# Kernel optimization log

Measured on AMD Instinct MI355X. Metric: run time of the kernel, lower is better.

## Reference

```python
import jax, jax.numpy as jnp
import numpy as np

N = 50000   # nodes
E = 600000  # edges
D = 128     # emb_dim
L = 5       # num_layers
ATOM_DIMS = np.array([119, 4, 11, 13, 11, 7, 13, 2, 9]) + 5   # per-feature vocab (+5 as in source)
BOND_DIMS = np.array([7, 22, 2]) + 5
BL_CENTERS = np.arange(0.0, 2.0, 0.1, dtype=np.float32)   # 20 centers, gamma 10
PR_CENTERS = np.arange(0.0, 1.0, 0.05, dtype=np.float32)  # 20 centers, gamma 1
BL_GAMMA = 10.0
PR_GAMMA = 1.0
BN_EPS = 1e-5


def setup_inputs() -> dict:
    key = jax.random.key(0)
    ks = jax.random.split(key, 16)
    scale = 1.0 / np.sqrt(D)
    atom_off = jnp.asarray(np.concatenate([[0], np.cumsum(ATOM_DIMS)[:-1]]), jnp.int32)
    bond_off = jnp.asarray(np.concatenate([[0], np.cumsum(BOND_DIMS)[:-1]]), jnp.int32)
    return {
        "x": jax.random.randint(ks[0], (N, 9), 0, 7, dtype=jnp.int32),
        "edge_index": jax.random.randint(ks[1], (2, E), 0, N, dtype=jnp.int32),
        "edge_attr_int": jax.random.randint(ks[2], (E, 3), 0, 7, dtype=jnp.int32),
        "edge_attr_float": jax.random.uniform(ks[3], (E, 2), dtype=jnp.float32),
        "atom_off": atom_off,
        "bond_off": bond_off,
        "atom_emb": jax.random.normal(ks[4], (int(ATOM_DIMS.sum()), D), jnp.float32) * scale,
        "bond_emb": jax.random.normal(ks[5], (L, int(BOND_DIMS.sum()), D), jnp.float32) * scale,
        "W_bl": jax.random.normal(ks[6], (L, len(BL_CENTERS), D), jnp.float32) * scale,
        "b_bl": jnp.zeros((L, D), jnp.float32),
        "W_pr": jax.random.normal(ks[7], (L, len(PR_CENTERS), D), jnp.float32) * scale,
        "b_pr": jnp.zeros((L, D), jnp.float32),
        "mlp_W1": jax.random.normal(ks[8], (L, D, D), jnp.float32) * scale,
        "mlp_b1": jnp.zeros((L, D), jnp.float32),
        "bn1_g": jnp.ones((L, D), jnp.float32),
        "bn1_b": jnp.zeros((L, D), jnp.float32),
        "mlp_W2": jax.random.normal(ks[9], (L, D, D), jnp.float32) * scale,
        "mlp_b2": jnp.zeros((L, D), jnp.float32),
        "eps_gin": jnp.zeros((L,), jnp.float32),
        "bn_g": jnp.ones((L, D), jnp.float32),
        "bn_b": jnp.zeros((L, D), jnp.float32),
    }


def _bn(h, g, b):
    # BatchNorm1d, training-mode batch statistics over the node axis
    m = h.mean(0)
    v = h.var(0)
    return (h - m) * jax.lax.rsqrt(v + BN_EPS) * g + b


def _rbf(x, centers, gamma):
    # exp(-gamma * (x - c)^2): [E] -> [E, n_centers]
    return jnp.exp(-gamma * jnp.square(x[:, None] - centers[None, :]))


def reference(x, edge_index, edge_attr_int, edge_attr_float, atom_off, bond_off,
              atom_emb, bond_emb, W_bl, b_bl, W_pr, b_pr,
              mlp_W1, mlp_b1, bn1_g, bn1_b, mlp_W2, mlp_b2,
              eps_gin, bn_g, bn_b):
    # AtomEncoder: sum of 9 categorical embeddings (flat table + offsets)
    h = atom_emb[x + atom_off[None, :]].sum(1)  # [N, D]
    src, dst = edge_index[0], edge_index[1]
    bl = _rbf(edge_attr_float[:, 0], jnp.asarray(BL_CENTERS), BL_GAMMA)  # [E, 20]
    pr = _rbf(edge_attr_float[:, 1], jnp.asarray(PR_CENTERS), PR_GAMMA)  # [E, 20]
    for l in range(L):
        # per-layer edge embedding: BondEncoder + BondFloatRBF
        e = bond_emb[l][edge_attr_int + bond_off[None, :]].sum(1)
        e = e + bl @ W_bl[l] + b_bl[l] + pr @ W_pr[l] + b_pr[l]
        # GINConv (aggr='add'): mlp((1+eps)*x + sum_j relu(x_j + e_ij))
        msg = jax.nn.relu(h[src] + e)                       # [E, D]
        agg = jax.ops.segment_sum(msg, dst, num_segments=N)  # [N, D]
        z = (1.0 + eps_gin[l]) * h + agg
        z = z @ mlp_W1[l] + mlp_b1[l]
        z = jax.nn.relu(_bn(z, bn1_g[l], bn1_b[l]))
        z = z @ mlp_W2[l] + mlp_b2[l]
        # outer per-layer BatchNorm; ReLU except last layer (drop_ratio=0)
        z = _bn(z, bn_g[l], bn_b[l])
        if l < L - 1:
            z = jax.nn.relu(z)
        h = z
    return h  # JK='last'
```

## Files before the change

### kernel.cpp

```cpp
#include <hip/hip_runtime.h>
#include <hip/hip_bf16.h>

#define GN 50000
#define GE 600000
#define DD 128
#define TQ 4096
#define NBOND 2268
#define TROWS (2*(TQ+1) + NBOND)
#define SCB 49
#define NBANK 64
#define SSET (NBANK*256)

typedef __attribute__((ext_vector_type(8))) short short8;
typedef __attribute__((ext_vector_type(4))) float floatx4;

__device__ __forceinline__ unsigned short f2b(float f) {
    __hip_bfloat16 h = __float2bfloat16(f);
    return __builtin_bit_cast(unsigned short, h);
}
__device__ __forceinline__ float b2f_lo(unsigned int u) { return __uint_as_float(u << 16); }
__device__ __forceinline__ float b2f_hi(unsigned int u) { return __uint_as_float(u & 0xffff0000u); }
__device__ __forceinline__ float bs2f(short s) {
    return __uint_as_float(((unsigned int)(unsigned short)s) << 16);
}

__global__ __launch_bounds__(256) void atom_kernel(
    const int* __restrict__ x, const int* __restrict__ atom_off,
    const float* __restrict__ atom_emb, unsigned short* __restrict__ h)
{
    int t = blockIdx.x * 256 + threadIdx.x;
    if (t >= GN * DD) return;
    int n = t >> 7, d = t & 127;
    float s = 0.f;
#pragma unroll
    for (int f = 0; f < 9; f++) {
        int idx = x[n * 9 + f] + atom_off[f];
        s += atom_emb[idx * DD + d];
    }
    h[t] = f2b(s);
}

__global__ __launch_bounds__(256) void hist_kernel(const int* __restrict__ ei, int* __restrict__ count)
{
    int e = blockIdx.x * 256 + threadIdx.x;
    if (e < GE) atomicAdd(&count[ei[GE + e]], 1);
}

__global__ __launch_bounds__(1024) void scan1_kernel(
    const int* __restrict__ count, int* __restrict__ row_start, int* __restrict__ blocksum)
{
    __shared__ int sh[1024];
    int t = threadIdx.x;
    int idx = blockIdx.x * 1024 + t;
    int v = (idx < GN) ? count[idx] : 0;
    sh[t] = v;
    __syncthreads();
    for (int off = 1; off < 1024; off <<= 1) {
        int u = (t >= off) ? sh[t - off] : 0;
        __syncthreads();
        sh[t] += u;
        __syncthreads();
    }
    if (idx <= GN) row_start[idx] = (t == 0) ? 0 : sh[t - 1];
    if (t == 1023) blocksum[blockIdx.x] = sh[1023];
}

__global__ __launch_bounds__(64) void scan2_kernel(
    const int* __restrict__ blocksum, int* __restrict__ blockoff)
{
    int t = threadIdx.x;
    int v = (t < SCB) ? blocksum[t] : 0;
#pragma unroll
    for (int off = 1; off < 64; off <<= 1) {
        int u = __shfl_up(v, off);
        if (t >= off) v += u;
    }
    int e = __shfl_up(v, 1);
    if (t == 0) e = 0;
    if (t < SCB) blockoff[t] = e;
}

__global__ __launch_bounds__(1024) void scan3_kernel(
    int* __restrict__ row_start, const int* __restrict__ blockoff)
{
    int idx = blockIdx.x * 1024 + threadIdx.x;
    if (idx <= GN) row_start[idx] += blockoff[blockIdx.x];
}

__global__ __launch_bounds__(256) void scatter_kernel(
    const int* __restrict__ ei, const int* __restrict__ eai, const float* __restrict__ eaf,
    const int* __restrict__ row_start, int* __restrict__ fill, int4* __restrict__ ep)
{
    int e = blockIdx.x * 256 + threadIdx.x;
    if (e < GE) {
        int d = ei[GE + e];
        int p = row_start[d] + atomicAdd(&fill[d], 1);
        int src = ei[e];
        float x1 = eaf[2 * e], x2 = eaf[2 * e + 1];
        int q1 = (int)(x1 * (float)TQ + 0.5f); q1 = min(max(q1, 0), TQ);
        int q2 = (int)(x2 * (float)TQ + 0.5f); q2 = min(max(q2, 0), TQ);
        int b0 = eai[3 * e], b1 = eai[3 * e + 1], b2 = eai[3 * e + 2];
        ep[p] = make_int4(src, q1 | (q2 << 16), (b0 * 27 + b1) * 7 + b2, 0);
    }
}

__global__ __launch_bounds__(128) void tables_kernel(
    const float* __restrict__ W_bl, const float* __restrict__ b_bl,
    const float* __restrict__ W_pr, const float* __restrict__ b_pr,
    const float* __restrict__ bond_emb, const int* __restrict__ bond_off,
    unsigned short* __restrict__ tbl_bl, unsigned short* __restrict__ tbl_pr,
    unsigned short* __restrict__ tbl_bond)
{
    int l = blockIdx.x / TROWS;
    int b = blockIdx.x % TROWS;
    int d = threadIdx.x;
    const float* W_bl_l = W_bl + (size_t)l * 20 * DD;
    const float* W_pr_l = W_pr + (size_t)l * 20 * DD;
    const float* bemb_l = bond_emb + (size_t)l * 46 * DD;
    if (b < (TQ + 1)) {
        float xq = b * (1.0f / TQ);
        float s = b_bl[(size_t)l * DD + d] + b_pr[(size_t)l * DD + d];
#pragma unroll
        for (int k = 0; k < 20; k++) {
            float dl = xq - 0.1f * k;
            s += __expf(-10.f * dl * dl) * W_bl_l[k * DD + d];
        }
        tbl_bl[((size_t)l * (TQ + 1) + b) * DD + d] = f2b(s);
    } else if (b < 2 * (TQ + 1)) {
        int q = b - (TQ + 1);
        float xq = q * (1.0f / TQ);
        float s = 0.f;
#pragma unroll
        for (int k = 0; k < 20; k++) {
            float dl = xq - 0.05f * k;
            s += __expf(-dl * dl) * W_pr_l[k * DD + d];
        }
        tbl_pr[((size_t)l * (TQ + 1) + q) * DD + d] = f2b(s);
    } else {
        int r = b - 2 * (TQ + 1);
        int b0 = r / 189;
        int rem = r % 189;
        int b1 = rem / 7, b2 = rem % 7;
        tbl_bond[((size_t)l * NBOND + r) * DD + d] =
            f2b(bemb_l[(b0 + bond_off[0]) * DD + d]
              + bemb_l[(b1 + bond_off[1]) * DD + d]
              + bemb_l[(b2 + bond_off[2]) * DD + d]);
    }
}

__global__ __launch_bounds__(256) void wfrag_kernel(
    const float* __restrict__ W1, const float* __restrict__ W2,
    unsigned short* __restrict__ wf_hi, unsigned short* __restrict__ wf_lo)
{
    int t = blockIdx.x * 256 + threadIdx.x;
    if (t >= 10 * 2048) return;
    int mat = t >> 11;
    int rem = t & 2047;
    int kt = rem >> 9;
    int rem2 = rem & 511;
    int nt = rem2 >> 6;
    int lane = rem2 & 63;
    const float* src = (mat & 1) ? (W2 + (size_t)(mat >> 1) * DD * DD)
                                 : (W1 + (size_t)(mat >> 1) * DD * DD);
    int n = nt * 16 + (lane & 15);
    int k0 = kt * 32 + (lane >> 4) * 8;
    size_t base = (size_t)mat * 16384 + (size_t)((kt * 8 + nt) * 64 + lane) * 8;
#pragma unroll
    for (int j = 0; j < 8; j++) {
        float w = src[(size_t)(k0 + j) * DD + n];
        unsigned short hi = f2b(w);
        wf_hi[base + j] = hi;
        wf_lo[base + j] = f2b(w - bs2f((short)hi));
    }
}

__global__ __launch_bounds__(256) void edge_kernel(
    const int4* __restrict__ ep,
    const unsigned short* __restrict__ tbl_bl, const unsigned short* __restrict__ tbl_pr,
    const unsigned short* __restrict__ tbl_bond,
    const unsigned short* __restrict__ h, const int* __restrict__ row_start,
    const float* __restrict__ eps_gin, int layer,
    float* __restrict__ A)
{
    int tid = threadIdx.x;
    int wid = __builtin_amdgcn_readfirstlane(tid >> 6);
    int lane = tid & 63;
    int n = blockIdx.x * 4 + wid;
    int s0 = __builtin_amdgcn_readfirstlane(row_start[n]);
    int s1 = __builtin_amdgcn_readfirstlane(row_start[n + 1]);
    const unsigned int* hu = (const unsigned int*)h;
    const unsigned int* tb = (const unsigned int*)tbl_bl;
    const unsigned int* tp = (const unsigned int*)tbl_pr;
    const unsigned int* tg = (const unsigned int*)tbl_bond;
    float a0 = 0.f, a1 = 0.f;
    int p = s0;
    for (; p + 2 <= s1; p += 2) {
        int4 m0 = ep[p];
        int4 m1 = ep[p + 1];
        unsigned int ub0 = tb[(size_t)(m0.y & 0xffff) * 64 + lane];
        unsigned int up0 = tp[(size_t)((unsigned)m0.y >> 16) * 64 + lane];
        unsigned int ug0 = tg[(size_t)m0.z * 64 + lane];
        unsigned int uh0 = hu[(size_t)m0.x * 64 + lane];
        unsigned int ub1 = tb[(size_t)(m1.y & 0xffff) * 64 + lane];
        unsigned int up1 = tp[(size_t)((unsigned)m1.y >> 16) * 64 + lane];
        unsigned int ug1 = tg[(size_t)m1.z * 64 + lane];
        unsigned int uh1 = hu[(size_t)m1.x * 64 + lane];
        a0 += fmaxf(b2f_lo(uh0) + b2f_lo(ub0) + b2f_lo(up0) + b2f_lo(ug0), 0.f);
        a1 += fmaxf(b2f_hi(uh0) + b2f_hi(ub0) + b2f_hi(up0) + b2f_hi(ug0), 0.f);
        a0 += fmaxf(b2f_lo(uh1) + b2f_lo(ub1) + b2f_lo(up1) + b2f_lo(ug1), 0.f);
        a1 += fmaxf(b2f_hi(uh1) + b2f_hi(ub1) + b2f_hi(up1) + b2f_hi(ug1), 0.f);
    }
    if (p < s1) {
        int4 m0 = ep[p];
        unsigned int ub0 = tb[(size_t)(m0.y & 0xffff) * 64 + lane];
        unsigned int up0 = tp[(size_t)((unsigned)m0.y >> 16) * 64 + lane];
        unsigned int ug0 = tg[(size_t)m0.z * 64 + lane];
        unsigned int uh0 = hu[(size_t)m0.x * 64 + lane];
        a0 += fmaxf(b2f_lo(uh0) + b2f_lo(ub0) + b2f_lo(up0) + b2f_lo(ug0), 0.f);
        a1 += fmaxf(b2f_hi(uh0) + b2f_hi(ub0) + b2f_hi(up0) + b2f_hi(ug0), 0.f);
    }
    float eps1 = 1.f + eps_gin[layer];
    unsigned int un = hu[(size_t)n * 64 + lane];
    a0 += eps1 * b2f_lo(un);
    a1 += eps1 * b2f_hi(un);
    float2 o; o.x = a0; o.y = a1;
    *(float2*)(A + (size_t)n * DD + 2 * lane) = o;
}

template <int MODE>
__global__ __launch_bounds__(256) void gemm_kernel(
    const float* __restrict__ Asrc,
    const unsigned short* __restrict__ wf_hi, const unsigned short* __restrict__ wf_lo,
    const float* __restrict__ bias, float* __restrict__ Cdst,
    const float* __restrict__ stats_in, const float* __restrict__ bn_g,
    const float* __restrict__ bn_b, float* __restrict__ stats_out)
{
    __shared__ float sc_s[DD], tr_s[DD];
    __shared__ float red_s[4][DD];
    __shared__ float red_q[4][DD];
    int tid = threadIdx.x, wid = tid >> 6, lane = tid & 63;
    if (MODE == 1) {
        if (tid < DD) {
            float s = 0.f, q = 0.f;
#pragma unroll
            for (int bk = 0; bk < NBANK; bk++) {
                s += stats_in[bk * 256 + tid];
                q += stats_in[bk * 256 + 128 + tid];
            }
            float m = s * (1.0f / GN);
            float v = q * (1.0f / GN) - m * m;
            float sc = bn_g[tid] * rsqrtf(v + 1e-5f);
            sc_s[tid] = sc;
            tr_s[tid] = bn_b[tid] - m * sc;
        }
        __syncthreads();
    }
    int quad = lane >> 4, l16 = lane & 15;
    int row = blockIdx.x * 64 + wid * 16 + l16;
    bool rvalid = row < GN;

    floatx4 acc[8];
#pragma unroll
    for (int nt = 0; nt < 8; nt++) acc[nt] = (floatx4){0.f, 0.f, 0.f, 0.f};

    const short8* bhp = (const short8*)wf_hi;
    const short8* blp = (const short8*)wf_lo;
#pragma unroll
    for (int kt = 0; kt < 4; kt++) {
        short8 ahi = {0,0,0,0,0,0,0,0}, alo = {0,0,0,0,0,0,0,0};
        if (rvalid) {
            const float* ap = Asrc + (size_t)row * DD + kt * 32 + quad * 8;
            float a[8];
            *(float4*)(a)     = *(const float4*)(ap);
            *(float4*)(a + 4) = *(const float4*)(ap + 4);
            if (MODE == 1) {
                int kb = kt * 32 + quad * 8;
#pragma unroll
                for (int j = 0; j < 8; j++)
                    a[j] = fmaxf(a[j] * sc_s[kb + j] + tr_s[kb + j], 0.f);
            }
#pragma unroll
            for (int j = 0; j < 8; j++) {
                unsigned short hi = f2b(a[j]);
                ahi[j] = (short)hi;
                alo[j] = (short)f2b(a[j] - bs2f((short)hi));
            }
        }
#pragma unroll
        for (int nt = 0; nt < 8; nt++) {
            short8 bhi = bhp[(kt * 8 + nt) * 64 + lane];
            short8 blo = blp[(kt * 8 + nt) * 64 + lane];
            acc[nt] = __builtin_amdgcn_mfma_f32_16x16x32_bf16(ahi, bhi, acc[nt], 0, 0, 0);
            acc[nt] = __builtin_amdgcn_mfma_f32_16x16x32_bf16(alo, bhi, acc[nt], 0, 0, 0);
            acc[nt] = __builtin_amdgcn_mfma_f32_16x16x32_bf16(ahi, blo, acc[nt], 0, 0, 0);
        }
    }

#pragma unroll
    for (int nt = 0; nt < 8; nt++) {
        int col = nt * 16 + l16;
        float bv = bias[col];
        float s = 0.f, q = 0.f;
#pragma unroll
        for (int v = 0; v < 4; v++) {
            int r = blockIdx.x * 64 + wid * 16 + quad * 4 + v;
            float o = acc[nt][v] + bv;
            if (r < GN) {
                s += o; q += o * o;
                Cdst[(size_t)r * DD + col] = o;
            }
        }
        s += __shfl_xor(s, 16); s += __shfl_xor(s, 32);
        q += __shfl_xor(q, 16); q += __shfl_xor(q, 32);
        if (lane < 16) { red_s[wid][col] = s; red_q[wid][col] = q; }
    }
    __syncthreads();
    int bank = blockIdx.x & (NBANK - 1);
    if (tid < DD) {
        float s = red_s[0][tid] + red_s[1][tid] + red_s[2][tid] + red_s[3][tid];
        atomicAdd(&stats_out[bank * 256 + tid], s);
    } else {
        int c = tid - DD;
        float q = red_q[0][c] + red_q[1][c] + red_q[2][c] + red_q[3][c];
        atomicAdd(&stats_out[bank * 256 + 128 + c], q);
    }
}

__global__ __launch_bounds__(256) void bn_apply_kernel(
    const float* __restrict__ Z, const float* __restrict__ stats2,
    const float* __restrict__ g, const float* __restrict__ b,
    unsigned short* __restrict__ hout, float* __restrict__ fout, int last)
{
    __shared__ float sc_s[DD], tr_s[DD];
    int tid = threadIdx.x;
    if (tid < DD) {
        float s = 0.f, q = 0.f;
#pragma unroll
        for (int bk = 0; bk < NBANK; bk++) {
            s += stats2[bk * 256 + tid];
            q += stats2[bk * 256 + 128 + tid];
        }
        float m = s * (1.0f / GN);
        float v = q * (1.0f / GN) - m * m;
        float sc = g[tid] * rsqrtf(v + 1e-5f);
        sc_s[tid] = sc;
        tr_s[tid] = b[tid] - m * sc;
    }
    __syncthreads();
    const int total = GN * DD;
    for (int t = blockIdx.x * 256 + tid; t < total; t += gridDim.x * 256) {
        int c = t & 127;
        float val = Z[t] * sc_s[c] + tr_s[c];
        if (last) fout[t] = val;
        else      hout[t] = f2b(fmaxf(val, 0.f));
    }
}

extern "C" void kernel_launch(void* const* d_in, const int* in_sizes, int n_in,
                              void* d_out, int out_size, void* d_ws, size_t ws_size,
                              hipStream_t stream)
{
    const int*   x        = (const int*)d_in[0];
    const int*   ei       = (const int*)d_in[1];
    const int*   eai      = (const int*)d_in[2];
    const float* eaf      = (const float*)d_in[3];
    const int*   atom_off = (const int*)d_in[4];
    const int*   bond_off = (const int*)d_in[5];
    const float* atom_emb = (const float*)d_in[6];
    const float* bond_emb = (const float*)d_in[7];
    const float* W_bl     = (const float*)d_in[8];
    const float* b_bl     = (const float*)d_in[9];
    const float* W_pr     = (const float*)d_in[10];
    const float* b_pr     = (const float*)d_in[11];
    const float* W1       = (const float*)d_in[12];
    const float* b1       = (const float*)d_in[13];
    const float* bn1g     = (const float*)d_in[14];
    const float* bn1b     = (const float*)d_in[15];
    const float* W2       = (const float*)d_in[16];
    const float* b2       = (const float*)d_in[17];
    const float* eps_gin  = (const float*)d_in[18];
    const float* bng      = (const float*)d_in[19];
    const float* bnb      = (const float*)d_in[20];
    float* out = (float*)d_out;

    char* p = (char*)d_ws;
    unsigned short* h_bf  = (unsigned short*)p;  p += (size_t)GN * DD * 2;
    float* A              = (float*)p;           p += (size_t)GN * DD * 4;
    float* z1             = (float*)p;           p += (size_t)GN * DD * 4;
    unsigned short* tbl_bl   = (unsigned short*)p;  p += (size_t)5 * (TQ + 1) * DD * 2;
    unsigned short* tbl_pr   = (unsigned short*)p;  p += (size_t)5 * (TQ + 1) * DD * 2;
    unsigned short* tbl_bond = (unsigned short*)p;  p += (size_t)5 * NBOND * DD * 2;
    unsigned short* wf_hi    = (unsigned short*)p;  p += (size_t)10 * 16384 * 2;
    unsigned short* wf_lo    = (unsigned short*)p;  p += (size_t)10 * 16384 * 2;
    float* stats_all = (float*)p;  p += (size_t)10 * SSET * 4;
    int* count    = (int*)p;    p += (size_t)GN * 4;
    int* fill     = (int*)p;    p += (size_t)GN * 4;
    int* row_start= (int*)p;    p += (size_t)(GN + 1) * 4;
    int* blocksum = (int*)p;    p += (size_t)SCB * 4;
    int* blockoff = (int*)p;    p += (size_t)SCB * 4;
    p = (char*)(((size_t)p + 15) & ~(size_t)15);
    int4* ep      = (int4*)p;   p += (size_t)GE * 16;

    hipMemsetAsync(count, 0, (size_t)GN * 4, stream);
    hipMemsetAsync(fill,  0, (size_t)GN * 4, stream);
    hipMemsetAsync(stats_all, 0, (size_t)10 * SSET * 4, stream);

    hist_kernel<<<(GE + 255) / 256, 256, 0, stream>>>(ei, count);
    scan1_kernel<<<SCB, 1024, 0, stream>>>(count, row_start, blocksum);
    scan2_kernel<<<1, 64, 0, stream>>>(blocksum, blockoff);
    scan3_kernel<<<SCB, 1024, 0, stream>>>(row_start, blockoff);
    scatter_kernel<<<(GE + 255) / 256, 256, 0, stream>>>(ei, eai, eaf, row_start, fill, ep);
    atom_kernel<<<(GN * DD + 255) / 256, 256, 0, stream>>>(x, atom_off, atom_emb, h_bf);
    wfrag_kernel<<<80, 256, 0, stream>>>(W1, W2, wf_hi, wf_lo);
    tables_kernel<<<5 * TROWS, 128, 0, stream>>>(
        W_bl, b_bl, W_pr, b_pr, bond_emb, bond_off, tbl_bl, tbl_pr, tbl_bond);

    for (int l = 0; l < 5; l++) {
        float* stats1 = stats_all + (size_t)(2 * l + 0) * SSET;
        float* stats2 = stats_all + (size_t)(2 * l + 1) * SSET;

        edge_kernel<<<GN / 4, 256, 0, stream>>>(
            ep,
            tbl_bl + (size_t)l * (TQ + 1) * DD,
            tbl_pr + (size_t)l * (TQ + 1) * DD,
            tbl_bond + (size_t)l * NBOND * DD,
            h_bf, row_start, eps_gin, l, A);

        gemm_kernel<0><<<(GN + 63) / 64, 256, 0, stream>>>(
            A, wf_hi + (size_t)(l * 2 + 0) * 16384, wf_lo + (size_t)(l * 2 + 0) * 16384,
            b1 + (size_t)l * DD, z1, nullptr, nullptr, nullptr, stats1);

        gemm_kernel<1><<<(GN + 63) / 64, 256, 0, stream>>>(
            z1, wf_hi + (size_t)(l * 2 + 1) * 16384, wf_lo + (size_t)(l * 2 + 1) * 16384,
            b2 + (size_t)l * DD, A,
            stats1, bn1g + (size_t)l * DD, bn1b + (size_t)l * DD, stats2);

        bn_apply_kernel<<<1024, 256, 0, stream>>>(
            A, stats2, bng + (size_t)l * DD, bnb + (size_t)l * DD,
            h_bf, out, (l == 4) ? 1 : 0);
    }
}
```

Measured before the change: 773.2 us.

## Fuse edge aggregation with first MLP GEMM via LDS-staged tile

Merges the per-node edge aggregation kernel and the first MLP GEMM into one kernel. Each 256-thread block aggregates 64 node rows into an LDS tile, then runs the split-bf16 MFMA GEMM on it, writes z1 and accumulates BN statistics. This removes the fp32 A round trip through global memory and one launch per layer. In exchange, each wave processes 16 nodes serially and the grid shrinks from 12500 to 782 blocks, which may lower the latency hiding available to the gather. NBANK drops from 64 to 16 and the templated gemm is simplified to its single remaining mode.

```diff
diff --git a/kernel.cpp b/kernel.cpp
--- a/kernel.cpp
+++ b/kernel.cpp
@@ -8,8 +8,10 @@
 #define NBOND 2268
 #define TROWS (2*(TQ+1) + NBOND)
 #define SCB 49
-#define NBANK 64
+#define NBANK 16
 #define SSET (NBANK*256)
+#define NB 782
+#define LDA 132
 
 typedef __attribute__((ext_vector_type(8))) short short8;
 typedef __attribute__((ext_vector_type(4))) float floatx4;
@@ -174,60 +176,130 @@
     }
 }
 
-__global__ __launch_bounds__(256) void edge_kernel(
+__global__ __launch_bounds__(256) void edge_gemm_kernel(
     const int4* __restrict__ ep,
     const unsigned short* __restrict__ tbl_bl, const unsigned short* __restrict__ tbl_pr,
     const unsigned short* __restrict__ tbl_bond,
     const unsigned short* __restrict__ h, const int* __restrict__ row_start,
     const float* __restrict__ eps_gin, int layer,
-    float* __restrict__ A)
-{
+    const unsigned short* __restrict__ wf_hi, const unsigned short* __restrict__ wf_lo,
+    const float* __restrict__ bias, float* __restrict__ Cdst, float* __restrict__ stats_out)
+{
+    __shared__ float At[64 * LDA];
+    __shared__ float red_s[4][DD];
+    __shared__ float red_q[4][DD];
     int tid = threadIdx.x;
     int wid = __builtin_amdgcn_readfirstlane(tid >> 6);
     int lane = tid & 63;
-    int n = blockIdx.x * 4 + wid;
-    int s0 = __builtin_amdgcn_readfirstlane(row_start[n]);
-    int s1 = __builtin_amdgcn_readfirstlane(row_start[n + 1]);
+
     const unsigned int* hu = (const unsigned int*)h;
     const unsigned int* tb = (const unsigned int*)tbl_bl;
     const unsigned int* tp = (const unsigned int*)tbl_pr;
     const unsigned int* tg = (const unsigned int*)tbl_bond;
-    float a0 = 0.f, a1 = 0.f;
-    int p = s0;
-    for (; p + 2 <= s1; p += 2) {
-        int4 m0 = ep[p];
-        int4 m1 = ep[p + 1];
-        unsigned int ub0 = tb[(size_t)(m0.y & 0xffff) * 64 + lane];
-        unsigned int up0 = tp[(size_t)((unsigned)m0.y >> 16) * 64 + lane];
-        unsigned int ug0 = tg[(size_t)m0.z * 64 + lane];
-        unsigned int uh0 = hu[(size_t)m0.x * 64 + lane];
-        unsigned int ub1 = tb[(size_t)(m1.y & 0xffff) * 64 + lane];
-        unsigned int up1 = tp[(size_t)((unsigned)m1.y >> 16) * 64 + lane];
-        unsigned int ug1 = tg[(size_t)m1.z * 64 + lane];
-        unsigned int uh1 = hu[(size_t)m1.x * 64 + lane];
-        a0 += fmaxf(b2f_lo(uh0) + b2f_lo(ub0) + b2f_lo(up0) + b2f_lo(ug0), 0.f);
-        a1 += fmaxf(b2f_hi(uh0) + b2f_hi(ub0) + b2f_hi(up0) + b2f_hi(ug0), 0.f);
-        a0 += fmaxf(b2f_lo(uh1) + b2f_lo(ub1) + b2f_lo(up1) + b2f_lo(ug1), 0.f);
-        a1 += fmaxf(b2f_hi(uh1) + b2f_hi(ub1) + b2f_hi(up1) + b2f_hi(ug1), 0.f);
-    }
-    if (p < s1) {
-        int4 m0 = ep[p];
-        unsigned int ub0 = tb[(size_t)(m0.y & 0xffff) * 64 + lane];
-        unsigned int up0 = tp[(size_t)((unsigned)m0.y >> 16) * 64 + lane];
-        unsigned int ug0 = tg[(size_t)m0.z * 64 + lane];
-        unsigned int uh0 = hu[(size_t)m0.x * 64 + lane];
-        a0 += fmaxf(b2f_lo(uh0) + b2f_lo(ub0) + b2f_lo(up0) + b2f_lo(ug0), 0.f);
-        a1 += fmaxf(b2f_hi(uh0) + b2f_hi(ub0) + b2f_hi(up0) + b2f_hi(ug0), 0.f);
-    }
     float eps1 = 1.f + eps_gin[layer];
-    unsigned int un = hu[(size_t)n * 64 + lane];
-    a0 += eps1 * b2f_lo(un);
-    a1 += eps1 * b2f_hi(un);
-    float2 o; o.x = a0; o.y = a1;
-    *(float2*)(A + (size_t)n * DD + 2 * lane) = o;
-}
-
-template <int MODE>
+    for (int i = 0; i < 16; i++) {
+        int rl = wid * 16 + i;
+        int n = blockIdx.x * 64 + rl;
+        float a0 = 0.f, a1 = 0.f;
+        if (n < GN) {
+            int s0 = __builtin_amdgcn_readfirstlane(row_start[n]);
+            int s1 = __builtin_amdgcn_readfirstlane(row_start[n + 1]);
+            int p = s0;
+            for (; p + 2 <= s1; p += 2) {
+                int4 m0 = ep[p];
+                int4 m1 = ep[p + 1];
+                unsigned int ub0 = tb[(size_t)(m0.y & 0xffff) * 64 + lane];
+                unsigned int up0 = tp[(size_t)((unsigned)m0.y >> 16) * 64 + lane];
+                unsigned int ug0 = tg[(size_t)m0.z * 64 + lane];
+                unsigned int uh0 = hu[(size_t)m0.x * 64 + lane];
+                unsigned int ub1 = tb[(size_t)(m1.y & 0xffff) * 64 + lane];
+                unsigned int up1 = tp[(size_t)((unsigned)m1.y >> 16) * 64 + lane];
+                unsigned int ug1 = tg[(size_t)m1.z * 64 + lane];
+                unsigned int uh1 = hu[(size_t)m1.x * 64 + lane];
+                a0 += fmaxf(b2f_lo(uh0) + b2f_lo(ub0) + b2f_lo(up0) + b2f_lo(ug0), 0.f);
+                a1 += fmaxf(b2f_hi(uh0) + b2f_hi(ub0) + b2f_hi(up0) + b2f_hi(ug0), 0.f);
+                a0 += fmaxf(b2f_lo(uh1) + b2f_lo(ub1) + b2f_lo(up1) + b2f_lo(ug1), 0.f);
+                a1 += fmaxf(b2f_hi(uh1) + b2f_hi(ub1) + b2f_hi(up1) + b2f_hi(ug1), 0.f);
+            }
+            if (p < s1) {
+                int4 m0 = ep[p];
+                unsigned int ub0 = tb[(size_t)(m0.y & 0xffff) * 64 + lane];
+                unsigned int up0 = tp[(size_t)((unsigned)m0.y >> 16) * 64 + lane];
+                unsigned int ug0 = tg[(size_t)m0.z * 64 + lane];
+                unsigned int uh0 = hu[(size_t)m0.x * 64 + lane];
+                a0 += fmaxf(b2f_lo(uh0) + b2f_lo(ub0) + b2f_lo(up0) + b2f_lo(ug0), 0.f);
+                a1 += fmaxf(b2f_hi(uh0) + b2f_hi(ub0) + b2f_hi(up0) + b2f_hi(ug0), 0.f);
+            }
+            unsigned int un = hu[(size_t)n * 64 + lane];
+            a0 += eps1 * b2f_lo(un);
+            a1 += eps1 * b2f_hi(un);
+        }
+        float2 o; o.x = a0; o.y = a1;
+        *(float2*)(&At[rl * LDA + 2 * lane]) = o;
+    }
+    __syncthreads();
+
+    int quad = lane >> 4, l16 = lane & 15;
+    int rl2 = wid * 16 + l16;
+    floatx4 acc[8];
+#pragma unroll
+    for (int nt = 0; nt < 8; nt++) acc[nt] = (floatx4){0.f, 0.f, 0.f, 0.f};
+
+    const short8* bhp = (const short8*)wf_hi;
+    const short8* blp = (const short8*)wf_lo;
+#pragma unroll
+    for (int kt = 0; kt < 4; kt++) {
+        const float* ap = At + rl2 * LDA + kt * 32 + quad * 8;
+        float a[8];
+        *(float4*)(a)     = *(const float4*)(ap);
+        *(float4*)(a + 4) = *(const float4*)(ap + 4);
+        short8 ahi, alo;
+#pragma unroll
+        for (int j = 0; j < 8; j++) {
+            unsigned short hi = f2b(a[j]);
+            ahi[j] = (short)hi;
+            alo[j] = (short)f2b(a[j] - bs2f((short)hi));
+        }
+#pragma unroll
+        for (int nt = 0; nt < 8; nt++) {
+            short8 bhi = bhp[(kt * 8 + nt) * 64 + lane];
+            short8 blo = blp[(kt * 8 + nt) * 64 + lane];
+            acc[nt] = __builtin_amdgcn_mfma_f32_16x16x32_bf16(ahi, bhi, acc[nt], 0, 0, 0);
+            acc[nt] = __builtin_amdgcn_mfma_f32_16x16x32_bf16(alo, bhi, acc[nt], 0, 0, 0);
+            acc[nt] = __builtin_amdgcn_mfma_f32_16x16x32_bf16(ahi, blo, acc[nt], 0, 0, 0);
+        }
+    }
+
+#pragma unroll
+    for (int nt = 0; nt < 8; nt++) {
+        int col = nt * 16 + l16;
+        float bv = bias[col];
+        float s = 0.f, q = 0.f;
+#pragma unroll
+        for (int v = 0; v < 4; v++) {
+            int r = blockIdx.x * 64 + wid * 16 + quad * 4 + v;
+            float o = acc[nt][v] + bv;
+            if (r < GN) {
+                s += o; q += o * o;
+                Cdst[(size_t)r * DD + col] = o;
+            }
+        }
+        s += __shfl_xor(s, 16); s += __shfl_xor(s, 32);
+        q += __shfl_xor(q, 16); q += __shfl_xor(q, 32);
+        if (lane < 16) { red_s[wid][col] = s; red_q[wid][col] = q; }
+    }
+    __syncthreads();
+    int bank = blockIdx.x & (NBANK - 1);
+    if (tid < DD) {
+        float s = red_s[0][tid] + red_s[1][tid] + red_s[2][tid] + red_s[3][tid];
+        atomicAdd(&stats_out[bank * 256 + tid], s);
+    } else {
+        int c = tid - DD;
+        float q = red_q[0][c] + red_q[1][c] + red_q[2][c] + red_q[3][c];
+        atomicAdd(&stats_out[bank * 256 + 128 + c], q);
+    }
+}
+
 __global__ __launch_bounds__(256) void gemm_kernel(
     const float* __restrict__ Asrc,
     const unsigned short* __restrict__ wf_hi, const unsigned short* __restrict__ wf_lo,
@@ -239,22 +311,20 @@
     __shared__ float red_s[4][DD];
     __shared__ float red_q[4][DD];
     int tid = threadIdx.x, wid = tid >> 6, lane = tid & 63;
-    if (MODE == 1) {
-        if (tid < DD) {
-            float s = 0.f, q = 0.f;
-#pragma unroll
-            for (int bk = 0; bk < NBANK; bk++) {
-                s += stats_in[bk * 256 + tid];
-                q += stats_in[bk * 256 + 128 + tid];
-            }
-            float m = s * (1.0f / GN);
-            float v = q * (1.0f / GN) - m * m;
-            float sc = bn_g[tid] * rsqrtf(v + 1e-5f);
-            sc_s[tid] = sc;
-            tr_s[tid] = bn_b[tid] - m * sc;
-        }
-        __syncthreads();
-    }
+    if (tid < DD) {
+        float s = 0.f, q = 0.f;
+#pragma unroll
+        for (int bk = 0; bk < NBANK; bk++) {
+            s += stats_in[bk * 256 + tid];
+            q += stats_in[bk * 256 + 128 + tid];
+        }
+        float m = s * (1.0f / GN);
+        float v = q * (1.0f / GN) - m * m;
+        float sc = bn_g[tid] * rsqrtf(v + 1e-5f);
+        sc_s[tid] = sc;
+        tr_s[tid] = bn_b[tid] - m * sc;
+    }
+    __syncthreads();
     int quad = lane >> 4, l16 = lane & 15;
     int row = blockIdx.x * 64 + wid * 16 + l16;
     bool rvalid = row < GN;
@@ -273,12 +343,10 @@
             float a[8];
             *(float4*)(a)     = *(const float4*)(ap);
             *(float4*)(a + 4) = *(const float4*)(ap + 4);
-            if (MODE == 1) {
-                int kb = kt * 32 + quad * 8;
-#pragma unroll
-                for (int j = 0; j < 8; j++)
-                    a[j] = fmaxf(a[j] * sc_s[kb + j] + tr_s[kb + j], 0.f);
-            }
+            int kb = kt * 32 + quad * 8;
+#pragma unroll
+            for (int j = 0; j < 8; j++)
+                a[j] = fmaxf(a[j] * sc_s[kb + j] + tr_s[kb + j], 0.f);
 #pragma unroll
             for (int j = 0; j < 8; j++) {
                 unsigned short hi = f2b(a[j]);
@@ -385,8 +453,8 @@
 
     char* p = (char*)d_ws;
     unsigned short* h_bf  = (unsigned short*)p;  p += (size_t)GN * DD * 2;
-    float* A              = (float*)p;           p += (size_t)GN * DD * 4;
     float* z1             = (float*)p;           p += (size_t)GN * DD * 4;
+    float* z2             = (float*)p;           p += (size_t)GN * DD * 4;
     unsigned short* tbl_bl   = (unsigned short*)p;  p += (size_t)5 * (TQ + 1) * DD * 2;
     unsigned short* tbl_pr   = (unsigned short*)p;  p += (size_t)5 * (TQ + 1) * DD * 2;
     unsigned short* tbl_bond = (unsigned short*)p;  p += (size_t)5 * NBOND * DD * 2;
@@ -419,24 +487,22 @@
         float* stats1 = stats_all + (size_t)(2 * l + 0) * SSET;
         float* stats2 = stats_all + (size_t)(2 * l + 1) * SSET;
 
-        edge_kernel<<<GN / 4, 256, 0, stream>>>(
+        edge_gemm_kernel<<<NB, 256, 0, stream>>>(
             ep,
             tbl_bl + (size_t)l * (TQ + 1) * DD,
             tbl_pr + (size_t)l * (TQ + 1) * DD,
             tbl_bond + (size_t)l * NBOND * DD,
-            h_bf, row_start, eps_gin, l, A);
-
-        gemm_kernel<0><<<(GN + 63) / 64, 256, 0, stream>>>(
-            A, wf_hi + (size_t)(l * 2 + 0) * 16384, wf_lo + (size_t)(l * 2 + 0) * 16384,
-            b1 + (size_t)l * DD, z1, nullptr, nullptr, nullptr, stats1);
-
-        gemm_kernel<1><<<(GN + 63) / 64, 256, 0, stream>>>(
+            h_bf, row_start, eps_gin, l,
+            wf_hi + (size_t)(l * 2 + 0) * 16384, wf_lo + (size_t)(l * 2 + 0) * 16384,
+            b1 + (size_t)l * DD, z1, stats1);
+
+        gemm_kernel<<<NB, 256, 0, stream>>>(
             z1, wf_hi + (size_t)(l * 2 + 1) * 16384, wf_lo + (size_t)(l * 2 + 1) * 16384,
-            b2 + (size_t)l * DD, A,
+            b2 + (size_t)l * DD, z2,
             stats1, bn1g + (size_t)l * DD, bn1b + (size_t)l * DD, stats2);
 
         bn_apply_kernel<<<1024, 256, 0, stream>>>(
-            A, stats2, bng + (size_t)l * DD, bnb + (size_t)l * DD,
+            z2, stats2, bng + (size_t)l * DD, bnb + (size_t)l * DD,
             h_bf, out, (l == 4) ? 1 : 0);
     }
 }
```

Result: slower. 1.163 ms (+50.4%).
